# Kernel tuning notes

Measured on AMD Instinct MI355X. Metric: run time of the kernel, lower is better.

## Reference

```python
import jax, jax.numpy as jnp
import numpy as np

N_FFT = 2048
HOP = 512
K = N_FFT // 2 + 1  # 1025 output frequency bins


def _dft_window_weights(n_fft):
    """Windowed real/imag DFT matrices, matching librosa hann (periodic) window
    and W[j,k] = exp(-2*pi*i*j*k/n_fft); conv weight = (W[:, :K] * win[:, None]).T."""
    n = np.arange(n_fft)
    win = 0.5 - 0.5 * np.cos(2.0 * np.pi * n / n_fft)  # hann, fftbins=True
    k = np.arange(n_fft // 2 + 1)
    ang = 2.0 * np.pi * np.outer(k, n) / n_fft  # (K, n_fft)
    w_real = np.cos(ang) * win[None, :]
    w_imag = -np.sin(ang) * win[None, :]
    return (jnp.asarray(w_real, jnp.float32), jnp.asarray(w_imag, jnp.float32))


def setup_inputs() -> dict:
    key = jax.random.key(0)
    x = jax.random.normal(key, (16, 2, 262144), dtype=jnp.float32)
    w_real, w_imag = _dft_window_weights(N_FFT)
    return {"x": x, "w_real": w_real, "w_imag": w_imag}


def reference(x, w_real, w_imag):
    B, C, L = x.shape
    pad = N_FFT // 2
    xp = jnp.pad(x, ((0, 0), (0, 0), (pad, pad)), mode="reflect")  # center=True
    T = (L + 2 * pad - N_FFT) // HOP + 1  # number of frames
    idx = HOP * jnp.arange(T)[:, None] + jnp.arange(N_FFT)[None, :]  # (T, n_fft)
    frames = xp[:, :, idx]  # (B, C, T, n_fft)
    # Windowed DFT as GEMM (same math as the conv-as-DFT in the torch module).
    real = jnp.einsum("bctn,kn->bckt", frames, w_real)  # (B, C, K, T)
    imag = jnp.einsum("bctn,kn->bckt", frames, w_imag)
    # torch.cat over channel dim -> (B, C*K, T), channel-major order
    real = real.reshape(B, C * K, T)
    imag = imag.reshape(B, C * K, T)
    return (real, imag)
```

## Files before the change

kernel.cpp:

```cpp
#include <hip/hip_runtime.h>

#define NFFT  2048
#define KF    1025
#define MROWS 2050
#define TT    513
#define HOPS  512
#define LSIG  262144
#define PADL  1024
#define XPADN 264192
#define XDN   66048
#define IMOFF (16 * MROWS * TT)
#define NBC   32

typedef __attribute__((ext_vector_type(8))) short bf16x8;
typedef __attribute__((ext_vector_type(4))) short bf16x4;
typedef __attribute__((ext_vector_type(4))) float f32x4;

__device__ __forceinline__ short f2bf(float f) {
    union { float f; unsigned u; } v; v.f = f;
    unsigned r = v.u + 0x7fffu + ((v.u >> 16) & 1u);
    return (short)(r >> 16);
}

typedef __attribute__((address_space(1))) void gas_void;
typedef __attribute__((address_space(3))) void las_void;

__device__ __forceinline__ void gload_lds16(const short* g, short* l) {
    __builtin_amdgcn_global_load_lds((gas_void*)(void*)const_cast<short*>(g),
                                     (las_void*)(void*)l, 16, 0, 0);
}

__global__ __launch_bounds__(256)
void prep_x(const float* __restrict__ x, short* __restrict__ xpad,
            short* __restrict__ xd) {
    const int bc = blockIdx.y;
    const int j4 = (blockIdx.x * 256 + threadIdx.x) * 4;
    const float* xb = x + (size_t)bc * LSIG;
    float4 v;
    if (j4 >= PADL && j4 + 4 <= PADL + LSIG) {
        v = *(const float4*)(xb + (j4 - PADL));
    } else {
        float t[4];
#pragma unroll
        for (int e = 0; e < 4; e++) {
            int s = j4 + e - PADL;
            if (s < 0) s = -s;
            if (s >= LSIG) s = 2 * LSIG - 2 - s;
            t[e] = xb[s];
        }
        v = make_float4(t[0], t[1], t[2], t[3]);
    }
    bf16x4 b = { f2bf(v.x), f2bf(v.y), f2bf(v.z), f2bf(v.w) };
    *(bf16x4*)(xpad + (size_t)bc * XPADN + j4) = b;
    const int j = j4 >> 2;
#pragma unroll
    for (int r = 0; r < 4; r++)
        xd[((size_t)r * NBC + bc) * XDN + j] = b[r];
}

__global__ __launch_bounds__(256)
void prep_basis2(const float* __restrict__ wr, const float* __restrict__ wi,
                 short* __restrict__ A) {
    const int r   = blockIdx.y;
    const int row = blockIdx.x;
    const float* w = ((row & 1) ? wi : wr) + (size_t)(row >> 1) * NFFT + r;
    short* dst = A + ((size_t)r * 512 + row) * 512;
    for (int m = threadIdx.x; m < 512; m += 256)
        dst[m] = f2bf(w[4 * m]);
}

__global__ __launch_bounds__(512, 4)
void stft_gemm_f(const short* __restrict__ Ab, const short* __restrict__ xd,
                 float* __restrict__ out) {
    __shared__ short As[2][128 * 64];
    __shared__ short Bs[2][64 * 64];

    const int tid   = threadIdx.x;
    const int bcg   = blockIdx.x;
    const int mBase = blockIdx.y * 128;
    const int t0    = blockIdx.z * 64;

    const int lane = tid & 63;
    const int wid  = tid >> 6;
    const int wm   = (wid >> 2) * 64;
    const int wn   = (wid & 3) * 16;
    const int l16  = lane & 15;
    const int quad = lane >> 4;

    const int lrow = lane >> 3;
    const int csrc = (lane & 7) ^ lrow;

    const int raw = 16 * wid;
    const int rbw = 8 * wid;
    int brw = t0 + rbw + lrow; if (brw > 515) brw = 515;

    f32x4 acc[4][4];
#pragma unroll
    for (int r = 0; r < 4; r++)
#pragma unroll
        for (int i = 0; i < 4; i++)
            acc[r][i] = (f32x4){0.f, 0.f, 0.f, 0.f};

    const int r7 = l16 & 7;

#pragma unroll
    for (int rp = 0; rp < 2; rp++) {
        const short* Ap0 = Ab + ((size_t)(2 * rp) * 512 + mBase + raw + lrow) * 512 + csrc * 8;
        const short* Ap1 = Ap0 + (size_t)512 * 512;
        const short* Bp0 = xd + ((size_t)(2 * rp) * NBC + bcg) * XDN
                              + (size_t)brw * 128 + csrc * 8;
        const short* Bp1 = Bp0 + (size_t)NBC * XDN;

        for (int kt = 0; kt < 512; kt += 64) {
            __syncthreads();
#pragma unroll
            for (int i = 0; i < 2; i++) {
                gload_lds16(Ap0 + i * (8 * 512) + kt, &As[0][(raw + 8 * i) * 64]);
                gload_lds16(Ap1 + i * (8 * 512) + kt, &As[1][(raw + 8 * i) * 64]);
            }
            gload_lds16(Bp0 + kt, &Bs[0][rbw * 64]);
            gload_lds16(Bp1 + kt, &Bs[1][rbw * 64]);
            __syncthreads();
#pragma unroll
            for (int rr2 = 0; rr2 < 2; rr2++) {
#pragma unroll
                for (int kk = 0; kk < 64; kk += 32) {
                    const int p = ((kk >> 5) * 4 + quad) ^ r7;
                    bf16x8 af[4], bfr;
#pragma unroll
                    for (int i = 0; i < 4; i++)
                        af[i] = *(const bf16x8*)(&As[rr2][(wm + i * 16 + l16) * 64 + p * 8]);
                    bfr = *(const bf16x8*)(&Bs[rr2][(wn + l16) * 64 + p * 8]);
#pragma unroll
                    for (int i = 0; i < 4; i++)
                        acc[2 * rp + rr2][i] = __builtin_amdgcn_mfma_f32_16x16x32_bf16(
                            af[i], bfr, acc[2 * rp + rr2][i], 0, 0, 0);
                }
            }
        }
    }

    float* oRe = out + (size_t)bcg * KF * TT;
    float* oIm = out + (size_t)IMOFF + (size_t)bcg * KF * TT;

    const int t = t0 + wn + l16;
    if (t < TT) {
#pragma unroll
        for (int i = 0; i < 4; i++) {
            const int rowb = mBase + wm + i * 16 + quad * 4;
#pragma unroll
            for (int h = 0; h < 2; h++) {
                const int kap = (rowb >> 1) + h;
                const float u0 = acc[0][i][2 * h], v0 = acc[0][i][2 * h + 1];
                const float u1 = acc[1][i][2 * h], v1 = acc[1][i][2 * h + 1];
                const float u2 = acc[2][i][2 * h], v2 = acc[2][i][2 * h + 1];
                const float u3 = acc[3][i][2 * h], v3 = acc[3][i][2 * h + 1];
                const float Eu = u0 + u2, Epu = u0 - u2;
                const float Ou = u1 + u3, Opu = u1 - u3;
                const float Ev = v0 + v2, Epv = v0 - v2;
                const float Ov = v1 + v3, Opv = v1 - v3;
                const size_t rA = (size_t)kap * TT + t;
                const size_t rB = (size_t)(kap + 512) * TT + t;
                const size_t rC = (size_t)(512 - kap) * TT + t;
                const size_t rD = (size_t)(1024 - kap) * TT + t;
                oRe[rA] = Eu + Ou;    oIm[rA] = Ev + Ov;
                oRe[rB] = Epu + Opv;  oIm[rB] = Epv - Opu;
                oRe[rC] = Epu - Opv;  oIm[rC] = -(Epv + Opu);
                oRe[rD] = Eu - Ou;    oIm[rD] = -(Ev - Ov);
            }
        }
    }
}

__global__ __launch_bounds__(256)
void stft_tail(const float* __restrict__ wr, const float* __restrict__ wi,
               const short* __restrict__ xpad, float* __restrict__ out) {
    const int tb  = blockIdx.x;
    const int bc  = blockIdx.y;
    const int tid = threadIdx.x;
    const int lane = tid & 63;
    const int wid  = tid >> 6;
    const int l16  = lane & 15;
    const int quad = lane >> 4;

    const int t0 = (tb * 4 + wid) * 16;
    const int ls = l16 & 3;
    const int k  = 256 + (ls & 1) * 512;
    const float* bp = ((ls & 2) ? wi : wr) + (size_t)k * NFFT + quad * 8;
    const int tr = min(t0 + l16, 512);
    const short* ap = xpad + (size_t)bc * XPADN + (size_t)tr * HOPS + quad * 8;
    f32x4 acc0 = {0.f, 0.f, 0.f, 0.f}, acc1 = {0.f, 0.f, 0.f, 0.f};
    for (int kt = 0; kt < NFFT; kt += 64) {
        bf16x8 a0 = *(const bf16x8*)(ap + kt);
        bf16x8 a1 = *(const bf16x8*)(ap + kt + 32);
        float4 f0 = *(const float4*)(bp + kt), f1 = *(const float4*)(bp + kt + 4);
        float4 g0 = *(const float4*)(bp + kt + 32), g1 = *(const float4*)(bp + kt + 36);
        bf16x8 b0 = { f2bf(f0.x), f2bf(f0.y), f2bf(f0.z), f2bf(f0.w),
                      f2bf(f1.x), f2bf(f1.y), f2bf(f1.z), f2bf(f1.w) };
        bf16x8 b1 = { f2bf(g0.x), f2bf(g0.y), f2bf(g0.z), f2bf(g0.w),
                      f2bf(g1.x), f2bf(g1.y), f2bf(g1.z), f2bf(g1.w) };
        acc0 = __builtin_amdgcn_mfma_f32_16x16x32_bf16(a0, b0, acc0, 0, 0, 0);
        acc1 = __builtin_amdgcn_mfma_f32_16x16x32_bf16(a1, b1, acc1, 0, 0, 0);
    }
    if (l16 < 4) {
        size_t base = ((ls & 2) ? (size_t)IMOFF : 0) + (size_t)(bc * KF + k) * TT;
#pragma unroll
        for (int rr = 0; rr < 4; rr++) {
            int t = t0 + quad * 4 + rr;
            if (t < TT) out[base + t] = acc0[rr] + acc1[rr];
        }
    }
}

extern "C" void kernel_launch(void* const* d_in, const int* in_sizes, int n_in,
                              void* d_out, int out_size, void* d_ws, size_t ws_size,
                              hipStream_t stream) {
    const float* x  = (const float*)d_in[0];
    const float* wr = (const float*)d_in[1];
    const float* wi = (const float*)d_in[2];
    float* out = (float*)d_out;

    char* ws = (char*)d_ws;
    short* xpad = (short*)ws;
    short* xd   = (short*)(ws + 16908288);
    short* Ab   = (short*)(ws + 33816576);

    prep_x<<<dim3(258, NBC), 256, 0, stream>>>(x, xpad, xd);
    prep_basis2<<<dim3(512, 4), 256, 0, stream>>>(wr, wi, Ab);
    stft_gemm_f<<<dim3(NBC, 4, 9), 512, 0, stream>>>(Ab, xd, out);
    stft_tail<<<dim3(9, NBC), 256, 0, stream>>>(wr, wi, xpad, out);
}
```

Before: 279.6 us.

## Double-buffer GEMM LDS tiles to overlap global loads with MFMA

The STFT GEMM main loop now walks the four polyphase sub-problems in sequence with a double-buffered LDS ping-pong. The next k-tile is issued through global_load_lds while the current tile feeds MFMA, so each iteration needs one barrier instead of two. Before, both sub-problems' tiles were loaded into LDS and then computed, with the loads fully exposed. The change trades the earlier two-at-a-time reuse of shared loads for prefetch overlap, and it also changes the B row clamp.

```diff
diff --git a/kernel.cpp b/kernel.cpp
--- a/kernel.cpp
+++ b/kernel.cpp
@@ -11,6 +11,8 @@
 #define XDN   66048
 #define IMOFF (16 * MROWS * TT)
 #define NBC   32
+#define APL   262144
+#define BPL   (NBC * XDN)
 
 typedef __attribute__((ext_vector_type(8))) short bf16x8;
 typedef __attribute__((ext_vector_type(4))) short bf16x4;
@@ -92,7 +94,10 @@
 
     const int raw = 16 * wid;
     const int rbw = 8 * wid;
-    int brw = t0 + rbw + lrow; if (brw > 515) brw = 515;
+    int brw = t0 + rbw + lrow; if (brw > 512) brw = 512;
+
+    const short* aBase = Ab + ((size_t)(mBase + raw + lrow)) * 512 + csrc * 8;
+    const short* bBase = xd + (size_t)bcg * XDN + (size_t)brw * 128 + csrc * 8;
 
     f32x4 acc[4][4];
 #pragma unroll
@@ -103,40 +108,42 @@
 
     const int r7 = l16 & 7;
 
-#pragma unroll
-    for (int rp = 0; rp < 2; rp++) {
-        const short* Ap0 = Ab + ((size_t)(2 * rp) * 512 + mBase + raw + lrow) * 512 + csrc * 8;
-        const short* Ap1 = Ap0 + (size_t)512 * 512;
-        const short* Bp0 = xd + ((size_t)(2 * rp) * NBC + bcg) * XDN
-                              + (size_t)brw * 128 + csrc * 8;
-        const short* Bp1 = Bp0 + (size_t)NBC * XDN;
-
+    gload_lds16(aBase,            &As[0][(raw + 0) * 64]);
+    gload_lds16(aBase + 8 * 512,  &As[0][(raw + 8) * 64]);
+    gload_lds16(bBase,            &Bs[0][rbw * 64]);
+    __syncthreads();
+
+#pragma unroll
+    for (int r = 0; r < 4; r++) {
+        const size_t aR = (size_t)r * APL;
+        const size_t bR = (size_t)r * BPL;
         for (int kt = 0; kt < 512; kt += 64) {
+            const int cur = (kt >> 6) & 1;
+            if (r < 3 || kt < 448) {
+                const size_t aN = (kt < 448) ? (aR + kt + 64) : (aR + APL);
+                const size_t bN = (kt < 448) ? (bR + kt + 64) : (bR + BPL);
+                short* Asn = As[cur ^ 1];
+                short* Bsn = Bs[cur ^ 1];
+                gload_lds16(aBase + aN,           &Asn[(raw + 0) * 64]);
+                gload_lds16(aBase + aN + 8 * 512, &Asn[(raw + 8) * 64]);
+                gload_lds16(bBase + bN,           &Bsn[rbw * 64]);
+            }
+            const short* Asc = As[cur];
+            const short* Bsc = Bs[cur];
+#pragma unroll
+            for (int kk = 0; kk < 64; kk += 32) {
+                const int p = ((kk >> 5) * 4 + quad) ^ r7;
+                bf16x8 af[4];
+#pragma unroll
+                for (int i = 0; i < 4; i++)
+                    af[i] = *(const bf16x8*)(Asc + (wm + i * 16 + l16) * 64 + p * 8);
+                const bf16x8 bfr = *(const bf16x8*)(Bsc + (wn + l16) * 64 + p * 8);
+#pragma unroll
+                for (int i = 0; i < 4; i++)
+                    acc[r][i] = __builtin_amdgcn_mfma_f32_16x16x32_bf16(
+                        af[i], bfr, acc[r][i], 0, 0, 0);
+            }
             __syncthreads();
-#pragma unroll
-            for (int i = 0; i < 2; i++) {
-                gload_lds16(Ap0 + i * (8 * 512) + kt, &As[0][(raw + 8 * i) * 64]);
-                gload_lds16(Ap1 + i * (8 * 512) + kt, &As[1][(raw + 8 * i) * 64]);
-            }
-            gload_lds16(Bp0 + kt, &Bs[0][rbw * 64]);
-            gload_lds16(Bp1 + kt, &Bs[1][rbw * 64]);
-            __syncthreads();
-#pragma unroll
-            for (int rr2 = 0; rr2 < 2; rr2++) {
-#pragma unroll
-                for (int kk = 0; kk < 64; kk += 32) {
-                    const int p = ((kk >> 5) * 4 + quad) ^ r7;
-                    bf16x8 af[4], bfr;
-#pragma unroll
-                    for (int i = 0; i < 4; i++)
-                        af[i] = *(const bf16x8*)(&As[rr2][(wm + i * 16 + l16) * 64 + p * 8]);
-                    bfr = *(const bf16x8*)(&Bs[rr2][(wn + l16) * 64 + p * 8]);
-#pragma unroll
-                    for (int i = 0; i < 4; i++)
-                        acc[2 * rp + rr2][i] = __builtin_amdgcn_mfma_f32_16x16x32_bf16(
-                            af[i], bfr, acc[2 * rp + rr2][i], 0, 0, 0);
-                }
-            }
         }
     }
 
```

New measurement: 293.8 us. 1.05x slower.

## Restructure STFT GEMM: per-wave residue strips, async double buffering, LDS-staged butterfly

Applied to the files above, without the earlier changes.

Each of the four waves now owns one of the four decimation residues and keeps a private 64x64 A and B strip in a large dynamic LDS allocation. The next k-tile is double-buffered with direct global-to-LDS loads and vmcnt waits instead of block-wide barriers. Accumulators are staged through LDS so the radix-4 butterfly combine is done across waves with coalesced stores along t. This removes the per-tile __syncthreads and redundant fragment loads, but cuts occupancy to one 256-thread block per CU with 128KB of LDS, and doubles the grid in M.

```diff
diff --git a/kernel.cpp b/kernel.cpp
--- a/kernel.cpp
+++ b/kernel.cpp
@@ -11,6 +11,7 @@
 #define XDN   66048
 #define IMOFF (16 * MROWS * TT)
 #define NBC   32
+#define APL   262144
 
 typedef __attribute__((ext_vector_type(8))) short bf16x8;
 typedef __attribute__((ext_vector_type(4))) short bf16x4;
@@ -69,105 +70,125 @@
         dst[m] = f2bf(w[4 * m]);
 }
 
-__global__ __launch_bounds__(512, 4)
+__global__ __launch_bounds__(256, 1)
 void stft_gemm_f(const short* __restrict__ Ab, const short* __restrict__ xd,
                  float* __restrict__ out) {
-    __shared__ short As[2][128 * 64];
-    __shared__ short Bs[2][64 * 64];
-
-    const int tid   = threadIdx.x;
-    const int bcg   = blockIdx.x;
-    const int mBase = blockIdx.y * 128;
+    extern __shared__ short lds[];
+
+    const int tid  = threadIdx.x;
+    const int lane = tid & 63;
+    const int r    = tid >> 6;
+    const int bcg  = blockIdx.x;
+    const int mBase = blockIdx.y * 64;
     const int t0    = blockIdx.z * 64;
 
-    const int lane = tid & 63;
-    const int wid  = tid >> 6;
-    const int wm   = (wid >> 2) * 64;
-    const int wn   = (wid & 3) * 16;
     const int l16  = lane & 15;
     const int quad = lane >> 4;
-
     const int lrow = lane >> 3;
     const int csrc = (lane & 7) ^ lrow;
-
-    const int raw = 16 * wid;
-    const int rbw = 8 * wid;
-    int brw = t0 + rbw + lrow; if (brw > 515) brw = 515;
+    const int r7   = l16 & 7;
+
+    short* strip = lds + r * 16384;
+
+    const short* aSrc = Ab + (size_t)r * APL + (size_t)(mBase + lrow) * 512 + csrc * 8;
+    const short* bPlane = xd + ((size_t)r * NBC + bcg) * XDN + csrc * 8;
+    const short* bSrc[8];
+#pragma unroll
+    for (int i = 0; i < 8; i++) {
+        int bt = t0 + 8 * i + lrow; if (bt > 512) bt = 512;
+        bSrc[i] = bPlane + (size_t)bt * 128;
+    }
 
     f32x4 acc[4][4];
 #pragma unroll
-    for (int r = 0; r < 4; r++)
-#pragma unroll
-        for (int i = 0; i < 4; i++)
-            acc[r][i] = (f32x4){0.f, 0.f, 0.f, 0.f};
-
-    const int r7 = l16 & 7;
-
-#pragma unroll
-    for (int rp = 0; rp < 2; rp++) {
-        const short* Ap0 = Ab + ((size_t)(2 * rp) * 512 + mBase + raw + lrow) * 512 + csrc * 8;
-        const short* Ap1 = Ap0 + (size_t)512 * 512;
-        const short* Bp0 = xd + ((size_t)(2 * rp) * NBC + bcg) * XDN
-                              + (size_t)brw * 128 + csrc * 8;
-        const short* Bp1 = Bp0 + (size_t)NBC * XDN;
-
-        for (int kt = 0; kt < 512; kt += 64) {
-            __syncthreads();
-#pragma unroll
-            for (int i = 0; i < 2; i++) {
-                gload_lds16(Ap0 + i * (8 * 512) + kt, &As[0][(raw + 8 * i) * 64]);
-                gload_lds16(Ap1 + i * (8 * 512) + kt, &As[1][(raw + 8 * i) * 64]);
+    for (int i = 0; i < 4; i++)
+#pragma unroll
+        for (int j = 0; j < 4; j++)
+            acc[i][j] = (f32x4){0.f, 0.f, 0.f, 0.f};
+
+#pragma unroll
+    for (int i = 0; i < 8; i++) {
+        gload_lds16(aSrc + i * 4096, strip + i * 512);
+        gload_lds16(bSrc[i],         strip + 8192 + i * 512);
+    }
+
+    for (int kt = 0; kt < 512; kt += 64) {
+        const int cur = (kt >> 6) & 1;
+        if (kt < 448) {
+            short* dA = strip + ((cur ^ 1) << 12);
+            short* dB = strip + 8192 + ((cur ^ 1) << 12);
+            const int ko = kt + 64;
+#pragma unroll
+            for (int i = 0; i < 8; i++) {
+                gload_lds16(aSrc + i * 4096 + ko, dA + i * 512);
+                gload_lds16(bSrc[i] + ko,         dB + i * 512);
             }
-            gload_lds16(Bp0 + kt, &Bs[0][rbw * 64]);
-            gload_lds16(Bp1 + kt, &Bs[1][rbw * 64]);
-            __syncthreads();
-#pragma unroll
-            for (int rr2 = 0; rr2 < 2; rr2++) {
-#pragma unroll
-                for (int kk = 0; kk < 64; kk += 32) {
-                    const int p = ((kk >> 5) * 4 + quad) ^ r7;
-                    bf16x8 af[4], bfr;
-#pragma unroll
-                    for (int i = 0; i < 4; i++)
-                        af[i] = *(const bf16x8*)(&As[rr2][(wm + i * 16 + l16) * 64 + p * 8]);
-                    bfr = *(const bf16x8*)(&Bs[rr2][(wn + l16) * 64 + p * 8]);
-#pragma unroll
-                    for (int i = 0; i < 4; i++)
-                        acc[2 * rp + rr2][i] = __builtin_amdgcn_mfma_f32_16x16x32_bf16(
-                            af[i], bfr, acc[2 * rp + rr2][i], 0, 0, 0);
-                }
-            }
-        }
-    }
+            asm volatile("s_waitcnt vmcnt(16)" ::: "memory");
+        } else {
+            asm volatile("s_waitcnt vmcnt(0)" ::: "memory");
+        }
+        __builtin_amdgcn_sched_barrier(0);
+        const short* Ac = strip + (cur << 12);
+        const short* Bc = strip + 8192 + (cur << 12);
+#pragma unroll
+        for (int kk = 0; kk < 2; kk++) {
+            const int p = (kk * 4 + quad) ^ r7;
+            bf16x8 af[4], bfr[4];
+#pragma unroll
+            for (int i = 0; i < 4; i++)
+                af[i] = *(const bf16x8*)(Ac + (i * 16 + l16) * 64 + p * 8);
+#pragma unroll
+            for (int j = 0; j < 4; j++)
+                bfr[j] = *(const bf16x8*)(Bc + (j * 16 + l16) * 64 + p * 8);
+#pragma unroll
+            for (int i = 0; i < 4; i++)
+#pragma unroll
+                for (int j = 0; j < 4; j++)
+                    acc[i][j] = __builtin_amdgcn_mfma_f32_16x16x32_bf16(
+                        af[i], bfr[j], acc[i][j], 0, 0, 0);
+        }
+    }
+
+    __syncthreads();
+    float* sf = (float*)lds;
+    float* Sr = sf + r * (64 * 66);
+#pragma unroll
+    for (int i = 0; i < 4; i++)
+#pragma unroll
+        for (int j = 0; j < 4; j++)
+#pragma unroll
+            for (int rr = 0; rr < 4; rr++)
+                Sr[(i * 16 + quad * 4 + rr) * 66 + j * 16 + l16] = acc[i][j][rr];
+    __syncthreads();
 
     float* oRe = out + (size_t)bcg * KF * TT;
     float* oIm = out + (size_t)IMOFF + (size_t)bcg * KF * TT;
-
-    const int t = t0 + wn + l16;
-    if (t < TT) {
-#pragma unroll
-        for (int i = 0; i < 4; i++) {
-            const int rowb = mBase + wm + i * 16 + quad * 4;
-#pragma unroll
-            for (int h = 0; h < 2; h++) {
-                const int kap = (rowb >> 1) + h;
-                const float u0 = acc[0][i][2 * h], v0 = acc[0][i][2 * h + 1];
-                const float u1 = acc[1][i][2 * h], v1 = acc[1][i][2 * h + 1];
-                const float u2 = acc[2][i][2 * h], v2 = acc[2][i][2 * h + 1];
-                const float u3 = acc[3][i][2 * h], v3 = acc[3][i][2 * h + 1];
-                const float Eu = u0 + u2, Epu = u0 - u2;
-                const float Ou = u1 + u3, Opu = u1 - u3;
-                const float Ev = v0 + v2, Epv = v0 - v2;
-                const float Ov = v1 + v3, Opv = v1 - v3;
-                const size_t rA = (size_t)kap * TT + t;
-                const size_t rB = (size_t)(kap + 512) * TT + t;
-                const size_t rC = (size_t)(512 - kap) * TT + t;
-                const size_t rD = (size_t)(1024 - kap) * TT + t;
-                oRe[rA] = Eu + Ou;    oIm[rA] = Ev + Ov;
-                oRe[rB] = Epu + Opv;  oIm[rB] = Epv - Opu;
-                oRe[rC] = Epu - Opv;  oIm[rC] = -(Epv + Opu);
-                oRe[rD] = Eu - Ou;    oIm[rD] = -(Ev - Ov);
-            }
+    const int tg = t0 + lane;
+    if (tg < TT) {
+#pragma unroll
+        for (int kl = 0; kl < 8; kl++) {
+            const int kap = r * 8 + kl;
+            const int kg  = (mBase >> 1) + kap;
+            float u0 = sf[0 * 4224 + (2 * kap) * 66 + lane];
+            float v0 = sf[0 * 4224 + (2 * kap + 1) * 66 + lane];
+            float u1 = sf[1 * 4224 + (2 * kap) * 66 + lane];
+            float v1 = sf[1 * 4224 + (2 * kap + 1) * 66 + lane];
+            float u2 = sf[2 * 4224 + (2 * kap) * 66 + lane];
+            float v2 = sf[2 * 4224 + (2 * kap + 1) * 66 + lane];
+            float u3 = sf[3 * 4224 + (2 * kap) * 66 + lane];
+            float v3 = sf[3 * 4224 + (2 * kap + 1) * 66 + lane];
+            const float Eu = u0 + u2, Epu = u0 - u2;
+            const float Ou = u1 + u3, Opu = u1 - u3;
+            const float Ev = v0 + v2, Epv = v0 - v2;
+            const float Ov = v1 + v3, Opv = v1 - v3;
+            const size_t rA = (size_t)kg * TT + tg;
+            const size_t rB = (size_t)(kg + 512) * TT + tg;
+            const size_t rC = (size_t)(512 - kg) * TT + tg;
+            const size_t rD = (size_t)(1024 - kg) * TT + tg;
+            oRe[rA] = Eu + Ou;    oIm[rA] = Ev + Ov;
+            oRe[rB] = Epu + Opv;  oIm[rB] = Epv - Opu;
+            oRe[rC] = Epu - Opv;  oIm[rC] = -(Epv + Opu);
+            oRe[rD] = Eu - Ou;    oIm[rD] = -(Ev - Ov);
         }
     }
 }
@@ -225,8 +246,16 @@
     short* xd   = (short*)(ws + 16908288);
     short* Ab   = (short*)(ws + 33816576);
 
+    static bool cfgDone = false;
+    if (!cfgDone) {
+        (void)hipFuncSetAttribute((const void*)stft_gemm_f,
+                                  hipFuncAttributeMaxDynamicSharedMemorySize,
+                                  131072);
+        cfgDone = true;
+    }
+
     prep_x<<<dim3(258, NBC), 256, 0, stream>>>(x, xpad, xd);
     prep_basis2<<<dim3(512, 4), 256, 0, stream>>>(wr, wi, Ab);
-    stft_gemm_f<<<dim3(NBC, 4, 9), 512, 0, stream>>>(Ab, xd, out);
+    stft_gemm_f<<<dim3(NBC, 8, 9), 256, 131072, stream>>>(Ab, xd, out);
     stft_tail<<<dim3(9, NBC), 256, 0, stream>>>(wr, wi, xpad, out);
 }
```

Result: slower. 293.4 us (+4.9%).
